# Kernel tuning notes

Measured on AMD Instinct MI355X. Metric: run time of the kernel, lower is better.

Reference implementation:

```python
import jax, jax.numpy as jnp
import numpy as np

D_MODEL = 512
D_FF = 2048
LN_EPS = 1e-5


def layer_norm(x, gamma, beta):
    mu = jnp.mean(x, axis=-1, keepdims=True)
    var = jnp.mean(jnp.square(x - mu), axis=-1, keepdims=True)
    return (x - mu) * jax.lax.rsqrt(var + LN_EPS) * gamma + beta


def setup_inputs() -> dict:
    key = jax.random.key(0)
    ks = jax.random.split(key, 8)
    B, S, D, F = 8, 2048, D_MODEL, D_FF
    s = 1.0 / np.sqrt(D)
    sf = 1.0 / np.sqrt(F)
    return {
        "x": jax.random.normal(ks[0], (B, S, D), dtype=jnp.float32),
        "Wq": jax.random.normal(ks[1], (D, D), dtype=jnp.float32) * s,
        "Wk": jax.random.normal(ks[2], (D, D), dtype=jnp.float32) * s,
        "Wv": jax.random.normal(ks[3], (D, D), dtype=jnp.float32) * s,
        "Wo": jax.random.normal(ks[4], (D, D), dtype=jnp.float32) * s,
        "W1": jax.random.normal(ks[5], (D, F), dtype=jnp.float32) * s,
        "b1": jnp.zeros((F,), dtype=jnp.float32),
        "W2": jax.random.normal(ks[6], (F, D), dtype=jnp.float32) * sf,
        "b2": jnp.zeros((D,), dtype=jnp.float32),
        "g1": jnp.ones((D,), dtype=jnp.float32),
        "be1": jnp.zeros((D,), dtype=jnp.float32),
        "g2": jnp.ones((D,), dtype=jnp.float32),
        "be2": jnp.zeros((D,), dtype=jnp.float32),
    }


def reference(x, Wq, Wk, Wv, Wo, W1, b1, W2, b2, g1, be1, g2, be2):
    # Attention block (single head, no causal mask)
    h = layer_norm(x, g1, be1)                       # [B,S,D]
    q = h @ Wq
    k = h @ Wk
    v = h @ Wv
    scale = 1.0 / jnp.sqrt(jnp.float32(x.shape[-1]))
    scores = jnp.einsum('bsd,btd->bst', q, k) * scale  # [B,S,S]
    p = jax.nn.softmax(scores, axis=-1)
    attn = jnp.einsum('bst,btd->bsd', p, v) @ Wo
    x = x + attn
    # MLP block
    h = layer_norm(x, g2, be2)
    return x + (jax.nn.gelu(h @ W1 + b1, approximate=False) @ W2 + b2)
```

## Files before the change

### kernel.cpp

```cpp
#include <hip/hip_runtime.h>
#include <math.h>

typedef __attribute__((ext_vector_type(8))) short short8;
typedef __attribute__((ext_vector_type(4))) float f32x4;

static __device__ __forceinline__ short f2bf(float f) {
  union { float f; unsigned u; } v; v.f = f;
  unsigned r = v.u + 0x7fffu + ((v.u >> 16) & 1u);
  return (short)(r >> 16);
}
static __device__ __forceinline__ float bf2f(short s) {
  union { unsigned u; float f; } v; v.u = ((unsigned)(unsigned short)s) << 16;
  return v.f;
}
static __device__ __forceinline__ float gelu_exact(float x) {
  return 0.5f * x * (1.0f + erff(x * 0.70710678118654752f));
}
static __device__ __forceinline__ f32x4 mfma16(short8 a, short8 b, f32x4 c) {
  return __builtin_amdgcn_mfma_f32_16x16x32_bf16(a, b, c, 0, 0, 0);
}
static __device__ __forceinline__ void gload16(const short* g, short* l) {
  __builtin_amdgcn_global_load_lds(
      (const __attribute__((address_space(1))) void*)g,
      (__attribute__((address_space(3))) void*)l, 16, 0, 0);
}

__global__ __launch_bounds__(256) void tcvt(const float* __restrict__ src,
                                            short* __restrict__ dst,
                                            int R, int C) {
  __shared__ float t[32][33];
  int c0 = blockIdx.x * 32, r0 = blockIdx.y * 32;
  int tx = threadIdx.x & 31, ty = threadIdx.x >> 5;
#pragma unroll
  for (int i = 0; i < 32; i += 8)
    t[ty + i][tx] = src[(long)(r0 + ty + i) * C + c0 + tx];
  __syncthreads();
#pragma unroll
  for (int i = 0; i < 32; i += 8)
    dst[(long)(c0 + ty + i) * R + r0 + tx] = f2bf(t[tx][ty + i]);
}

__global__ __launch_bounds__(256) void ln_kernel(const float* __restrict__ x,
                                                 const float* __restrict__ gamma,
                                                 const float* __restrict__ beta,
                                                 short* __restrict__ out) {
  int row = blockIdx.x * 4 + (threadIdx.x >> 6);
  int lane = threadIdx.x & 63;
  const float* xr = x + (long)row * 512 + lane * 8;
  float v[8];
  *(f32x4*)&v[0] = *(const f32x4*)&xr[0];
  *(f32x4*)&v[4] = *(const f32x4*)&xr[4];
  float s = 0.f, ss = 0.f;
#pragma unroll
  for (int i = 0; i < 8; i++) { s += v[i]; ss += v[i] * v[i]; }
#pragma unroll
  for (int off = 1; off < 64; off <<= 1) {
    s += __shfl_xor(s, off);
    ss += __shfl_xor(ss, off);
  }
  float mu = s * (1.0f / 512.0f);
  float var = ss * (1.0f / 512.0f) - mu * mu;
  float rstd = rsqrtf(var + 1e-5f);
  float gv[8], bv[8];
  *(f32x4*)&gv[0] = *(const f32x4*)&gamma[lane * 8];
  *(f32x4*)&gv[4] = *(const f32x4*)&gamma[lane * 8 + 4];
  *(f32x4*)&bv[0] = *(const f32x4*)&beta[lane * 8];
  *(f32x4*)&bv[4] = *(const f32x4*)&beta[lane * 8 + 4];
  short8 o;
#pragma unroll
  for (int i = 0; i < 8; i++) o[i] = f2bf((v[i] - mu) * rstd * gv[i] + bv[i]);
  *(short8*)(out + (long)row * 512 + lane * 8) = o;
}

__global__ __launch_bounds__(256) void softmax_kernel(short* __restrict__ sb) {
  int row = blockIdx.x * 4 + (threadIdx.x >> 6);
  int lane = threadIdx.x & 63;
  short* p = sb + (long)row * 2048;
  float v[32];
#pragma unroll
  for (int c = 0; c < 4; c++) {
    short8 raw = *(const short8*)&p[(c * 64 + lane) * 8];
#pragma unroll
    for (int k = 0; k < 8; k++) v[c * 8 + k] = bf2f(raw[k]);
  }
  float mx = v[0];
#pragma unroll
  for (int i = 1; i < 32; i++) mx = fmaxf(mx, v[i]);
#pragma unroll
  for (int off = 1; off < 64; off <<= 1) mx = fmaxf(mx, __shfl_xor(mx, off));
  float sum = 0.f;
#pragma unroll
  for (int i = 0; i < 32; i++) { v[i] = __expf(v[i] - mx); sum += v[i]; }
#pragma unroll
  for (int off = 1; off < 64; off <<= 1) sum += __shfl_xor(sum, off);
  float inv = 1.0f / sum;
#pragma unroll
  for (int c = 0; c < 4; c++) {
    short8 o;
#pragma unroll
    for (int k = 0; k < 8; k++) o[k] = f2bf(v[c * 8 + k] * inv);
    *(short8*)&p[(c * 64 + lane) * 8] = o;
  }
}

template <int EPI>
__global__ __launch_bounds__(256) void gemm_bt(
    const short* __restrict__ A0, const short* __restrict__ BT0,
    const int M, const int N, const int K,
    short* __restrict__ Cb, float* __restrict__ Cf,
    const float* __restrict__ bias, const float* __restrict__ resid,
    const float scale,
    const long sA, const long sB, const long sC) {
  __shared__ __align__(16) short As[128 * 32];
  __shared__ __align__(16) short Bs[128 * 32];

  const int z = blockIdx.z;
  const short* A = A0 + (long)z * sA;
  const short* BT = BT0 + (long)z * sB;

  const int m0 = blockIdx.y * 128, n0 = blockIdx.x * 128;
  const int tid = threadIdx.x;
  const int lane = tid & 63;
  const int wave = tid >> 6;
  const int r = lane & 15, g = lane >> 4;
  const int wm = (wave >> 1) * 64, wn = (wave & 1) * 64;

  const int rowa = tid >> 2;
  const int cola = (tid & 3) * 8;
  const short* gA = A + (long)(m0 + rowa) * K + cola;
  const short* gA2 = gA + (long)64 * K;
  const short* gB = BT + (long)(n0 + rowa) * K + cola;
  const short* gB2 = gB + (long)64 * K;
  short* lA = &As[rowa * 32 + cola];
  short* lA2 = &As[(rowa + 64) * 32 + cola];
  short* lB = &Bs[rowa * 32 + cola];
  short* lB2 = &Bs[(rowa + 64) * 32 + cola];

  f32x4 acc[4][4] = {};

  for (int k0 = 0; k0 < K; k0 += 32) {
    gload16(gA + k0, lA);
    gload16(gA2 + k0, lA2);
    gload16(gB + k0, lB);
    gload16(gB2 + k0, lB2);
    __syncthreads();
    short8 av[4], bv[4];
#pragma unroll
    for (int i = 0; i < 4; i++)
      av[i] = *(const short8*)&As[(wm + i * 16 + r) * 32 + g * 8];
#pragma unroll
    for (int j = 0; j < 4; j++)
      bv[j] = *(const short8*)&Bs[(wn + j * 16 + r) * 32 + g * 8];
#pragma unroll
    for (int i = 0; i < 4; i++)
#pragma unroll
      for (int j = 0; j < 4; j++)
        acc[i][j] = mfma16(av[i], bv[j], acc[i][j]);
    __syncthreads();
  }

#pragma unroll
  for (int i = 0; i < 4; i++)
#pragma unroll
    for (int j = 0; j < 4; j++) {
      const int mb = m0 + wm + i * 16 + g * 4;
      const int nn = n0 + wn + j * 16 + r;
#pragma unroll
      for (int q = 0; q < 4; q++) {
        const int mm = mb + q;
        const float val = acc[i][j][q];
        if (EPI == 0) {
          Cb[(long)z * sC + (long)mm * N + nn] = f2bf(val);
        } else if (EPI == 1) {
          Cb[(long)z * sC + (long)mm * N + nn] = f2bf(val * scale);
        } else if (EPI == 2) {
          Cb[(long)(mm >> 11) * (512 * 2048) + (long)nn * 2048 + (mm & 2047)] =
              f2bf(val);
        } else if (EPI == 3) {
          float vv = val + (bias ? bias[nn] : 0.0f) + resid[(long)mm * N + nn];
          Cf[(long)mm * N + nn] = vv;
        } else if (EPI == 4) {
          Cb[(long)mm * N + nn] = f2bf(gelu_exact(val + bias[nn]));
        }
      }
    }
}

extern "C" void kernel_launch(void* const* d_in, const int* in_sizes, int n_in,
                              void* d_out, int out_size, void* d_ws,
                              size_t ws_size, hipStream_t stream) {
  const float* x   = (const float*)d_in[0];
  const float* Wq  = (const float*)d_in[1];
  const float* Wk  = (const float*)d_in[2];
  const float* Wv  = (const float*)d_in[3];
  const float* Wo  = (const float*)d_in[4];
  const float* W1  = (const float*)d_in[5];
  const float* b1  = (const float*)d_in[6];
  const float* W2  = (const float*)d_in[7];
  const float* b2  = (const float*)d_in[8];
  const float* g1  = (const float*)d_in[9];
  const float* be1 = (const float*)d_in[10];
  const float* g2  = (const float*)d_in[11];
  const float* be2 = (const float*)d_in[12];
  float* out = (float*)d_out;

  char* w = (char*)d_ws;
  auto alloc = [&](size_t bytes) {
    char* p = w;
    w += (bytes + 255) & ~(size_t)255;
    return p;
  };
  short* WqT = (short*)alloc(512 * 512 * 2);
  short* WkT = (short*)alloc(512 * 512 * 2);
  short* WvT = (short*)alloc(512 * 512 * 2);
  short* WoT = (short*)alloc(512 * 512 * 2);
  short* W1T = (short*)alloc(2048L * 512 * 2);
  short* W2T = (short*)alloc(512L * 2048 * 2);
  short* hb  = (short*)alloc(16384L * 512 * 2);
  short* qb  = (short*)alloc(16384L * 512 * 2);
  short* kb  = (short*)alloc(16384L * 512 * 2);
  short* vT  = (short*)alloc(16384L * 512 * 2);
  float* x2  = (float*)alloc(16384L * 512 * 4);
  short* big = (short*)alloc(16384L * 2048 * 2);
  short* sb = big;
  short* ffb = big;
  short* attnb = qb;
  short* h2b = hb;

  const float scale = 0.044194173824159216f;

  tcvt<<<dim3(16, 16), 256, 0, stream>>>(Wq, WqT, 512, 512);
  tcvt<<<dim3(16, 16), 256, 0, stream>>>(Wk, WkT, 512, 512);
  tcvt<<<dim3(16, 16), 256, 0, stream>>>(Wv, WvT, 512, 512);
  tcvt<<<dim3(16, 16), 256, 0, stream>>>(Wo, WoT, 512, 512);
  tcvt<<<dim3(64, 16), 256, 0, stream>>>(W1, W1T, 512, 2048);
  tcvt<<<dim3(16, 64), 256, 0, stream>>>(W2, W2T, 2048, 512);

  ln_kernel<<<4096, 256, 0, stream>>>(x, g1, be1, hb);

  gemm_bt<0><<<dim3(4, 128), 256, 0, stream>>>(hb, WqT, 16384, 512, 512, qb,
                                               nullptr, nullptr, nullptr, 0.f,
                                               0, 0, 0);
  gemm_bt<0><<<dim3(4, 128), 256, 0, stream>>>(hb, WkT, 16384, 512, 512, kb,
                                               nullptr, nullptr, nullptr, 0.f,
                                               0, 0, 0);
  gemm_bt<2><<<dim3(4, 128), 256, 0, stream>>>(hb, WvT, 16384, 512, 512, vT,
                                               nullptr, nullptr, nullptr, 0.f,
                                               0, 0, 0);

  gemm_bt<1><<<dim3(16, 16, 8), 256, 0, stream>>>(
      qb, kb, 2048, 2048, 512, sb, nullptr, nullptr, nullptr, scale,
      2048L * 512, 2048L * 512, 2048L * 2048);

  softmax_kernel<<<4096, 256, 0, stream>>>(sb);

  gemm_bt<0><<<dim3(4, 16, 8), 256, 0, stream>>>(
      sb, vT, 2048, 512, 2048, attnb, nullptr, nullptr, nullptr, 0.f,
      2048L * 2048, 512L * 2048, 2048L * 512);

  gemm_bt<3><<<dim3(4, 128), 256, 0, stream>>>(attnb, WoT, 16384, 512, 512,
                                               nullptr, x2, nullptr, x, 0.f,
                                               0, 0, 0);

  ln_kernel<<<4096, 256, 0, stream>>>(x2, g2, be2, h2b);

  gemm_bt<4><<<dim3(16, 128), 256, 0, stream>>>(h2b, W1T, 16384, 2048, 512,
                                                ffb, nullptr, b1, nullptr, 0.f,
                                                0, 0, 0);

  gemm_bt<3><<<dim3(4, 128), 256, 0, stream>>>(ffb, W2T, 16384, 512, 2048,
                                               nullptr, out, b2, x2, 0.f,
                                               0, 0, 0);
}
```

Baseline: 416.4 us.

## Double-buffer GEMM LDS tiles and fuse Q/K/V projections into one GEMM

The GEMM main loop now uses two LDS buffers, so the global-to-LDS load for the next K-tile is issued before the MFMAs on the current tile, with one barrier per iteration instead of two. The three Q/K/V projection GEMMs are merged into a single launch against a concatenated [1536x512] transposed weight. A new epilogue routes columns to q, k, or transposed v, which cuts launch count and rereads of the LayerNorm output. LDS use doubles to 32KB per block, which may lower occupancy.

```diff
diff --git a/kernel.cpp b/kernel.cpp
--- a/kernel.cpp
+++ b/kernel.cpp
@@ -107,12 +107,13 @@
 __global__ __launch_bounds__(256) void gemm_bt(
     const short* __restrict__ A0, const short* __restrict__ BT0,
     const int M, const int N, const int K,
-    short* __restrict__ Cb, float* __restrict__ Cf,
+    short* __restrict__ Cb, short* __restrict__ Cb2, short* __restrict__ Cb3,
+    float* __restrict__ Cf,
     const float* __restrict__ bias, const float* __restrict__ resid,
     const float scale,
     const long sA, const long sB, const long sC) {
-  __shared__ __align__(16) short As[128 * 32];
-  __shared__ __align__(16) short Bs[128 * 32];
+  __shared__ __align__(16) short As[2][128 * 32];
+  __shared__ __align__(16) short Bs[2][128 * 32];
 
   const int z = blockIdx.z;
   const short* A = A0 + (long)z * sA;
@@ -131,32 +132,41 @@
   const short* gA2 = gA + (long)64 * K;
   const short* gB = BT + (long)(n0 + rowa) * K + cola;
   const short* gB2 = gB + (long)64 * K;
-  short* lA = &As[rowa * 32 + cola];
-  short* lA2 = &As[(rowa + 64) * 32 + cola];
-  short* lB = &Bs[rowa * 32 + cola];
-  short* lB2 = &Bs[(rowa + 64) * 32 + cola];
+  const int loff = rowa * 32 + cola;
+  const int loff2 = (rowa + 64) * 32 + cola;
 
   f32x4 acc[4][4] = {};
-
-  for (int k0 = 0; k0 < K; k0 += 32) {
-    gload16(gA + k0, lA);
-    gload16(gA2 + k0, lA2);
-    gload16(gB + k0, lB);
-    gload16(gB2 + k0, lB2);
-    __syncthreads();
+  const int nt = K >> 5;
+
+  gload16(gA, &As[0][loff]);
+  gload16(gA2, &As[0][loff2]);
+  gload16(gB, &Bs[0][loff]);
+  gload16(gB2, &Bs[0][loff2]);
+  __syncthreads();
+
+  int cur = 0;
+  for (int t = 0; t < nt; ++t) {
+    if (t + 1 < nt) {
+      const int k0 = (t + 1) << 5;
+      gload16(gA + k0, &As[cur ^ 1][loff]);
+      gload16(gA2 + k0, &As[cur ^ 1][loff2]);
+      gload16(gB + k0, &Bs[cur ^ 1][loff]);
+      gload16(gB2 + k0, &Bs[cur ^ 1][loff2]);
+    }
     short8 av[4], bv[4];
 #pragma unroll
     for (int i = 0; i < 4; i++)
-      av[i] = *(const short8*)&As[(wm + i * 16 + r) * 32 + g * 8];
+      av[i] = *(const short8*)&As[cur][(wm + i * 16 + r) * 32 + g * 8];
 #pragma unroll
     for (int j = 0; j < 4; j++)
-      bv[j] = *(const short8*)&Bs[(wn + j * 16 + r) * 32 + g * 8];
+      bv[j] = *(const short8*)&Bs[cur][(wn + j * 16 + r) * 32 + g * 8];
 #pragma unroll
     for (int i = 0; i < 4; i++)
 #pragma unroll
       for (int j = 0; j < 4; j++)
         acc[i][j] = mfma16(av[i], bv[j], acc[i][j]);
     __syncthreads();
+    cur ^= 1;
   }
 
 #pragma unroll
@@ -173,14 +183,21 @@
           Cb[(long)z * sC + (long)mm * N + nn] = f2bf(val);
         } else if (EPI == 1) {
           Cb[(long)z * sC + (long)mm * N + nn] = f2bf(val * scale);
-        } else if (EPI == 2) {
-          Cb[(long)(mm >> 11) * (512 * 2048) + (long)nn * 2048 + (mm & 2047)] =
-              f2bf(val);
         } else if (EPI == 3) {
           float vv = val + (bias ? bias[nn] : 0.0f) + resid[(long)mm * N + nn];
           Cf[(long)mm * N + nn] = vv;
         } else if (EPI == 4) {
           Cb[(long)mm * N + nn] = f2bf(gelu_exact(val + bias[nn]));
+        } else if (EPI == 5) {
+          const int sel = nn >> 9, c = nn & 511;
+          if (sel == 0) {
+            Cb[(long)mm * 512 + c] = f2bf(val);
+          } else if (sel == 1) {
+            Cb2[(long)mm * 512 + c] = f2bf(val);
+          } else {
+            Cb3[(long)(mm >> 11) * (512 * 2048) + (long)c * 2048 +
+                (mm & 2047)] = f2bf(val);
+          }
         }
       }
     }
@@ -210,9 +227,7 @@
     w += (bytes + 255) & ~(size_t)255;
     return p;
   };
-  short* WqT = (short*)alloc(512 * 512 * 2);
-  short* WkT = (short*)alloc(512 * 512 * 2);
-  short* WvT = (short*)alloc(512 * 512 * 2);
+  short* WqkvT = (short*)alloc(1536L * 512 * 2);
   short* WoT = (short*)alloc(512 * 512 * 2);
   short* W1T = (short*)alloc(2048L * 512 * 2);
   short* W2T = (short*)alloc(512L * 2048 * 2);
@@ -229,46 +244,40 @@
 
   const float scale = 0.044194173824159216f;
 
-  tcvt<<<dim3(16, 16), 256, 0, stream>>>(Wq, WqT, 512, 512);
-  tcvt<<<dim3(16, 16), 256, 0, stream>>>(Wk, WkT, 512, 512);
-  tcvt<<<dim3(16, 16), 256, 0, stream>>>(Wv, WvT, 512, 512);
+  tcvt<<<dim3(16, 16), 256, 0, stream>>>(Wq, WqkvT, 512, 512);
+  tcvt<<<dim3(16, 16), 256, 0, stream>>>(Wk, WqkvT + 512L * 512, 512, 512);
+  tcvt<<<dim3(16, 16), 256, 0, stream>>>(Wv, WqkvT + 1024L * 512, 512, 512);
   tcvt<<<dim3(16, 16), 256, 0, stream>>>(Wo, WoT, 512, 512);
   tcvt<<<dim3(64, 16), 256, 0, stream>>>(W1, W1T, 512, 2048);
   tcvt<<<dim3(16, 64), 256, 0, stream>>>(W2, W2T, 2048, 512);
 
   ln_kernel<<<4096, 256, 0, stream>>>(x, g1, be1, hb);
 
-  gemm_bt<0><<<dim3(4, 128), 256, 0, stream>>>(hb, WqT, 16384, 512, 512, qb,
-                                               nullptr, nullptr, nullptr, 0.f,
-                                               0, 0, 0);
-  gemm_bt<0><<<dim3(4, 128), 256, 0, stream>>>(hb, WkT, 16384, 512, 512, kb,
-                                               nullptr, nullptr, nullptr, 0.f,
-                                               0, 0, 0);
-  gemm_bt<2><<<dim3(4, 128), 256, 0, stream>>>(hb, WvT, 16384, 512, 512, vT,
-                                               nullptr, nullptr, nullptr, 0.f,
-                                               0, 0, 0);
+  gemm_bt<5><<<dim3(12, 128), 256, 0, stream>>>(
+      hb, WqkvT, 16384, 1536, 512, qb, kb, vT, nullptr, nullptr, nullptr, 0.f,
+      0, 0, 0);
 
   gemm_bt<1><<<dim3(16, 16, 8), 256, 0, stream>>>(
-      qb, kb, 2048, 2048, 512, sb, nullptr, nullptr, nullptr, scale,
-      2048L * 512, 2048L * 512, 2048L * 2048);
+      qb, kb, 2048, 2048, 512, sb, nullptr, nullptr, nullptr, nullptr, nullptr,
+      scale, 2048L * 512, 2048L * 512, 2048L * 2048);
 
   softmax_kernel<<<4096, 256, 0, stream>>>(sb);
 
   gemm_bt<0><<<dim3(4, 16, 8), 256, 0, stream>>>(
-      sb, vT, 2048, 512, 2048, attnb, nullptr, nullptr, nullptr, 0.f,
-      2048L * 2048, 512L * 2048, 2048L * 512);
-
-  gemm_bt<3><<<dim3(4, 128), 256, 0, stream>>>(attnb, WoT, 16384, 512, 512,
-                                               nullptr, x2, nullptr, x, 0.f,
-                                               0, 0, 0);
+      sb, vT, 2048, 512, 2048, attnb, nullptr, nullptr, nullptr, nullptr,
+      nullptr, 0.f, 2048L * 2048, 512L * 2048, 2048L * 512);
+
+  gemm_bt<3><<<dim3(4, 128), 256, 0, stream>>>(
+      attnb, WoT, 16384, 512, 512, nullptr, nullptr, nullptr, x2, nullptr, x,
+      0.f, 0, 0, 0);
 
   ln_kernel<<<4096, 256, 0, stream>>>(x2, g2, be2, h2b);
 
-  gemm_bt<4><<<dim3(16, 128), 256, 0, stream>>>(h2b, W1T, 16384, 2048, 512,
-                                                ffb, nullptr, b1, nullptr, 0.f,
-                                                0, 0, 0);
-
-  gemm_bt<3><<<dim3(4, 128), 256, 0, stream>>>(ffb, W2T, 16384, 512, 2048,
-                                               nullptr, out, b2, x2, 0.f,
-                                               0, 0, 0);
-}
+  gemm_bt<4><<<dim3(16, 128), 256, 0, stream>>>(
+      h2b, W1T, 16384, 2048, 512, ffb, nullptr, nullptr, nullptr, b1, nullptr,
+      0.f, 0, 0, 0);
+
+  gemm_bt<3><<<dim3(4, 128), 256, 0, stream>>>(
+      ffb, W2T, 16384, 512, 2048, nullptr, nullptr, nullptr, out, b2, x2, 0.f,
+      0, 0, 0);
+}
```

After: 409.9 us. No clear change (-1.6%).
